# Performance work log

Measured on AMD Instinct MI355X. Metric: run time of the kernel, lower is better.

## Reference

```python
import jax, jax.numpy as jnp
import numpy as np

B, D_MODEL, C, T = 2, 256, 64, 1024
N_HEADS = 8
EPS = 1e-5


def setup_inputs() -> dict:
    key = jax.random.key(0)
    k1, k2, k3 = jax.random.split(key, 3)
    x = jax.random.normal(k1, (B, D_MODEL, C, T), dtype=jnp.float32)
    in_w = jax.random.normal(k2, (3 * D_MODEL, D_MODEL), dtype=jnp.float32) * 0.05
    in_b = jnp.zeros((3 * D_MODEL,), jnp.float32)
    out_w = jax.random.normal(k3, (D_MODEL, D_MODEL), dtype=jnp.float32) * 0.05
    out_b = jnp.zeros((D_MODEL,), jnp.float32)
    return dict(x=x, in_w=in_w, in_b=in_b, out_w=out_w, out_b=out_b)


def reference(x, in_w, in_b, out_w, out_b):
    b, d, c, t = x.shape
    h = N_HEADS
    f = d // h
    scale = 1.0 / np.sqrt(f).astype(np.float32)

    # InstanceNorm2d (no affine): normalize each (b, channel) over spatial (c, t)
    mu = x.mean(axis=(2, 3), keepdims=True)
    var = x.var(axis=(2, 3), keepdims=True)  # biased, as torch
    xn = (x - mu) / jnp.sqrt(var + EPS)

    # 1x1 conv d -> 3d
    qkv = jnp.einsum('bdct,ed->bect', xn, in_w) + in_b[None, :, None, None]
    q, k, v = jnp.split(qkv, 3, axis=1)

    def to_heads(u):
        # b (h f) c t -> (b c) h f t
        u = u.reshape(b, h, f, c, t)
        u = u.transpose(0, 3, 1, 2, 4)
        return u.reshape(b * c, h, f, t)

    q = jax.nn.softmax(to_heads(q), axis=-2) * scale  # softmax over feature dim
    k = jax.nn.softmax(to_heads(k), axis=-1)          # softmax over length dim
    v = to_heads(v) / t

    # context: [n, h, f_k, f_v]
    ctx = jnp.einsum('nhkl,nhvl->nhkv', k, v)
    out = jnp.einsum('nhdv,nhdl->nhvl', ctx, q)

    # (b c) h f t -> b (h f) c t
    out = out.reshape(b, c, h, f, t).transpose(0, 2, 3, 1, 4).reshape(b, d, c, t)

    out = jnp.einsum('bdct,ed->bect', out, out_w) + out_b[None, :, None, None]
    return out + x
```

## Files before the change

kernel.cpp:

```cpp
#include <hip/hip_runtime.h>
#include <stdint.h>

#define D_MODEL 256
#define TDIM    1024
#define NHEADS  8
#define FDIM    32
#define P_LEN   65536
#define K3      768
#define BK      64

using u16 = unsigned short;

typedef __bf16 bf16x8 __attribute__((ext_vector_type(8)));
typedef float  floatx4 __attribute__((ext_vector_type(4)));

__device__ __forceinline__ float b2f(u16 u) {
    union { float f; uint32_t i; } v; v.i = ((uint32_t)u) << 16; return v.f;
}
__device__ __forceinline__ float b2f_lo(uint32_t u) {
    union { float f; uint32_t i; } v; v.i = u << 16; return v.f;
}
__device__ __forceinline__ float b2f_hi(uint32_t u) {
    union { float f; uint32_t i; } v; v.i = u & 0xffff0000u; return v.f;
}
__device__ __forceinline__ u16 f2b(float f) {
    union { float f; uint32_t i; } v; v.f = f;
    uint32_t i = v.i;
    uint32_t r = i + 0x7fffu + ((i >> 16) & 1u);
    return (u16)(r >> 16);
}
__device__ __forceinline__ uint32_t pack2(float lo, float hi) {
    return ((uint32_t)f2b(hi) << 16) | (uint32_t)f2b(lo);
}

__device__ __forceinline__ void gload_lds16(const u16* g, u16* l) {
    __builtin_amdgcn_global_load_lds((const __attribute__((address_space(1))) void*)g,
                                     (__attribute__((address_space(3))) void*)l,
                                     16, 0, 0);
}

__device__ __forceinline__ void stc(u16* p, float v) { *p = f2b(v); }
__device__ __forceinline__ void stc(float* p, float v) { *p = v; }

__global__ __launch_bounds__(256) void stats_kernel(const float* __restrict__ x,
                                                    float* __restrict__ mu,
                                                    float* __restrict__ rstd) {
    int bd = blockIdx.x;
    const float* row = x + (size_t)bd * P_LEN;
    int tid = threadIdx.x;
    float s = 0.f, sq = 0.f;
    for (int i = 0; i < P_LEN / (256 * 4); ++i) {
        int idx = (i * 256 + tid) * 4;
        float4 u = *(const float4*)(row + idx);
        s += u.x + u.y + u.z + u.w;
        sq += u.x * u.x + u.y * u.y + u.z * u.z + u.w * u.w;
    }
    for (int off = 32; off; off >>= 1) { s += __shfl_down(s, off); sq += __shfl_down(sq, off); }
    __shared__ float rs[4], rq[4];
    if ((tid & 63) == 0) { rs[tid >> 6] = s; rq[tid >> 6] = sq; }
    __syncthreads();
    if (tid == 0) {
        float S = rs[0] + rs[1] + rs[2] + rs[3];
        float Q = rq[0] + rq[1] + rq[2] + rq[3];
        float m = S * (1.f / 65536.f);
        float var = Q * (1.f / 65536.f) - m * m;
        mu[bd] = m;
        rstd[bd] = rsqrtf(var + 1e-5f);
    }
}

__global__ __launch_bounds__(256) void fold_kernel(const float* __restrict__ in_w,
                                                   const float* __restrict__ in_b,
                                                   const float* __restrict__ mu,
                                                   const float* __restrict__ rstd,
                                                   u16* __restrict__ Wp,
                                                   float* __restrict__ bprime) {
    int bid = blockIdx.x;
    int b = bid / K3, e = bid % K3;
    int d = threadIdx.x;
    float w = in_w[e * D_MODEL + d];
    float r = rstd[b * D_MODEL + d];
    float m = mu[b * D_MODEL + d];
    Wp[(size_t)bid * D_MODEL + d] = f2b(w * r);
    float contrib = w * r * m;
    for (int off = 32; off; off >>= 1) contrib += __shfl_down(contrib, off);
    __shared__ float rr[4];
    if ((d & 63) == 0) rr[d >> 6] = contrib;
    __syncthreads();
    if (d == 0) bprime[bid] = in_b[e] - (rr[0] + rr[1] + rr[2] + rr[3]);
}

__global__ __launch_bounds__(256) void transpose_x(const float* __restrict__ x,
                                                   u16* __restrict__ xt) {
    __shared__ float tile[64][65];
    int p0 = blockIdx.x * 64;
    int d0 = blockIdx.y * 64;
    int tid = threadIdx.x;
    int dr = tid >> 4;
    int pc = (tid & 15) * 4;
#pragma unroll
    for (int it = 0; it < 4; ++it) {
        int d = it * 16 + dr;
        float4 v = *(const float4*)&x[(size_t)(d0 + d) * P_LEN + p0 + pc];
        tile[pc + 0][d] = v.x;
        tile[pc + 1][d] = v.y;
        tile[pc + 2][d] = v.z;
        tile[pc + 3][d] = v.w;
    }
    __syncthreads();
    int pr = tid >> 3;
    int dc = (tid & 7) * 8;
#pragma unroll
    for (int it = 0; it < 2; ++it) {
        int p = it * 32 + pr;
        ushort4 o0 = make_ushort4(f2b(tile[p][dc + 0]), f2b(tile[p][dc + 1]),
                                  f2b(tile[p][dc + 2]), f2b(tile[p][dc + 3]));
        ushort4 o1 = make_ushort4(f2b(tile[p][dc + 4]), f2b(tile[p][dc + 5]),
                                  f2b(tile[p][dc + 6]), f2b(tile[p][dc + 7]));
        u16* dst = xt + (size_t)(p0 + p) * D_MODEL + d0 + dc;
        *(ushort4*)dst = o0;
        *(ushort4*)(dst + 4) = o1;
    }
}

template <bool RESID, bool PERC, typename OT>
__global__ __launch_bounds__(256) void mgemm(const u16* __restrict__ A,
                                             const u16* __restrict__ Bt,
                                             const float* __restrict__ bias,
                                             const float* __restrict__ resid,
                                             OT* __restrict__ Cout) {
    __shared__ __align__(16) u16 As[128 * BK];
    __shared__ __align__(16) u16 Bs[128 * BK];
    const int tid  = threadIdx.x;
    const int wave = tid >> 6;
    const int lane = tid & 63;
    const int m0 = blockIdx.y * 128;
    const int p0 = blockIdx.x * 128;
    const int mw = (wave >> 1) * 64;
    const int nw = (wave & 1) * 64;

    const u16* Ab = PERC ? A + ((size_t)(blockIdx.x >> 3) << 16) : A;

    floatx4 acc[4][4];
#pragma unroll
    for (int i = 0; i < 4; ++i)
#pragma unroll
        for (int j = 0; j < 4; ++j) acc[i][j] = (floatx4){0.f, 0.f, 0.f, 0.f};

    const int srow = lane >> 3;
    const int schunk = lane & 7;
    const int q  = lane >> 4;
    const int rl = lane & 15;

    for (int s = 0; s < 4; ++s) {
        const int k0 = s * BK;
#pragma unroll
        for (int j = 0; j < 4; ++j) {
            int rbase = wave * 32 + j * 8;
            int r = rbase + srow;
            int cg = schunk ^ (r & 7);
            gload_lds16(Ab + ((size_t)(m0 + r) << 8) + k0 + cg * 8, &As[rbase * BK]);
            gload_lds16(Bt + ((size_t)(p0 + r) << 8) + k0 + cg * 8, &Bs[rbase * BK]);
        }
        __syncthreads();
#pragma unroll
        for (int ks = 0; ks < 2; ++ks) {
            bf16x8 af[4], bf[4];
#pragma unroll
            for (int ti = 0; ti < 4; ++ti) {
                int r = mw + 16 * ti + rl;
                int cp = (ks * 4 + q) ^ (r & 7);
                af[ti] = *(const bf16x8*)&As[r * BK + cp * 8];
            }
#pragma unroll
            for (int tj = 0; tj < 4; ++tj) {
                int r = nw + 16 * tj + rl;
                int cp = (ks * 4 + q) ^ (r & 7);
                bf[tj] = *(const bf16x8*)&Bs[r * BK + cp * 8];
            }
#pragma unroll
            for (int ti = 0; ti < 4; ++ti)
#pragma unroll
                for (int tj = 0; tj < 4; ++tj)
                    acc[ti][tj] = __builtin_amdgcn_mfma_f32_16x16x32_bf16(
                        af[ti], bf[tj], acc[ti][tj], 0, 0, 0);
        }
        __syncthreads();
    }

#pragma unroll
    for (int ti = 0; ti < 4; ++ti) {
#pragma unroll
        for (int i = 0; i < 4; ++i) {
            int e = m0 + mw + 16 * ti + 4 * q + i;
            float bv = bias[e];
            size_t rowbase = (size_t)e * P_LEN + p0 + nw;
#pragma unroll
            for (int tj = 0; tj < 4; ++tj) {
                size_t addr = rowbase + 16 * tj + rl;
                float v = acc[ti][tj][i] + bv;
                if (RESID) v += resid[addr];
                stc(Cout + addr, v);
            }
        }
    }
}

__global__ __launch_bounds__(256) void qsm_kernel(const u16* __restrict__ qkv,
                                                  u16* __restrict__ pq) {
    int tid = threadIdx.x;
    int pair = tid >> 2;
    int hq = tid & 3;
    size_t p = (size_t)blockIdx.x * 128 + (size_t)pair * 2;
    const u16* qb = qkv + p;
#pragma unroll
    for (int hi = 0; hi < 2; ++hi) {
        int h = hq * 2 + hi;
        const u16* qh = qb + (size_t)(h * FDIM) * P_LEN;
        float a[32], b[32];
#pragma unroll
        for (int f = 0; f < 32; ++f) {
            uint32_t uu = *(const uint32_t*)(qh + (size_t)f * P_LEN);
            a[f] = __expf(b2f_lo(uu));
            b[f] = __expf(b2f_hi(uu));
        }
        float sa = 0.f, sb = 0.f;
#pragma unroll
        for (int f = 0; f < 32; ++f) { sa += a[f]; sb += b[f]; }
        sa = 1.f / sa; sb = 1.f / sb;
        u16* o1 = pq + p * D_MODEL + h * FDIM;
        u16* o2 = o1 + D_MODEL;
#pragma unroll
        for (int c = 0; c < 4; ++c) {
            union { u16 u[8]; uint4 v4; } pka, pkb;
#pragma unroll
            for (int i = 0; i < 8; ++i) {
                pka.u[i] = f2b(a[c * 8 + i] * sa);
                pkb.u[i] = f2b(b[c * 8 + i] * sb);
            }
            *(uint4*)(o1 + c * 8) = pka.v4;
            *(uint4*)(o2 + c * 8) = pkb.v4;
        }
    }
}

__global__ __launch_bounds__(256) void ctx_kernel(const u16* __restrict__ qkv,
                                                  float* __restrict__ ctx) {
    int bid = blockIdx.x;
    int c = bid >> 3, h = bid & 7;
    int tid = threadIdx.x;
    size_t colbase = (size_t)c * TDIM;
    const u16* kb = qkv + (size_t)(D_MODEL + h * FDIM) * P_LEN + colbase;
    const u16* vb = qkv + (size_t)(2 * D_MODEL + h * FDIM) * P_LEN + colbase;

    __shared__ float kinv[32];
    __shared__ __align__(16) u16 ekt[32 * 264];
    __shared__ __align__(16) u16 vsb[32 * 264];

    {
        int row = tid >> 3, g = tid & 7;
        const u16* krow = kb + (size_t)row * P_LEN;
        float s = 0.f;
#pragma unroll
        for (int i = 0; i < 16; ++i) {
            uint4 u = *(const uint4*)(krow + g * 8 + i * 64);
            s += __expf(b2f_lo(u.x)) + __expf(b2f_hi(u.x))
               + __expf(b2f_lo(u.y)) + __expf(b2f_hi(u.y))
               + __expf(b2f_lo(u.z)) + __expf(b2f_hi(u.z))
               + __expf(b2f_lo(u.w)) + __expf(b2f_hi(u.w));
        }
        for (int off = 4; off; off >>= 1) s += __shfl_down(s, off, 8);
        if (g == 0) kinv[row] = 0.17677669529663687f / (s * 1024.f);
    }
    __syncthreads();

    const int lane = tid & 63;
    const int wave = tid >> 6;
    const int rl = lane & 15, q = lane >> 4;
    const int mi = wave >> 1, ni = wave & 1;
    const int o  = tid & 31;
    const int r8 = tid >> 5;
    floatx4 acc = {0.f, 0.f, 0.f, 0.f};

    for (int ch = 0; ch < 4; ++ch) {
        int t0 = ch * 256;
        if (ch) __syncthreads();
#pragma unroll
        for (int pass = 0; pass < 4; ++pass) {
            int r = pass * 8 + r8;
            float iv = kinv[r];
            uint4 u = *((const uint4*)(kb + (size_t)r * P_LEN + t0) + o);
            uint4 w = *((const uint4*)(vb + (size_t)r * P_LEN + t0) + o);
            uint4 E;
            E.x = pack2(__expf(b2f_lo(u.x)) * iv, __expf(b2f_hi(u.x)) * iv);
            E.y = pack2(__expf(b2f_lo(u.y)) * iv, __expf(b2f_hi(u.y)) * iv);
            E.z = pack2(__expf(b2f_lo(u.z)) * iv, __expf(b2f_hi(u.z)) * iv);
            E.w = pack2(__expf(b2f_lo(u.w)) * iv, __expf(b2f_hi(u.w)) * iv);
            *(uint4*)&ekt[r * 264 + o * 8] = E;
            *(uint4*)&vsb[r * 264 + o * 8] = w;
        }
        __syncthreads();
#pragma unroll
        for (int ks = 0; ks < 8; ++ks) {
            bf16x8 a  = *(const bf16x8*)&ekt[(16 * mi + rl) * 264 + ks * 32 + q * 8];
            bf16x8 bv = *(const bf16x8*)&vsb[(16 * ni + rl) * 264 + ks * 32 + q * 8];
            acc = __builtin_amdgcn_mfma_f32_16x16x32_bf16(a, bv, acc, 0, 0, 0);
        }
    }

    float* co = ctx + (size_t)bid * 1024;
#pragma unroll
    for (int i = 0; i < 4; ++i)
        co[(16 * mi + 4 * q + i) * 32 + 16 * ni + rl] = acc[i];
}

__global__ __launch_bounds__(256) void wfold_kernel(const float* __restrict__ w2,
                                                    const float* __restrict__ ctx,
                                                    u16* __restrict__ w2p) {
    __shared__ float cs[8192];
    int c = blockIdx.x;
    int tid = threadIdx.x;
    const float4* cb = (const float4*)(ctx + (size_t)c * 8192);
#pragma unroll
    for (int i = 0; i < 8; ++i)
        ((float4*)cs)[i * 256 + tid] = cb[i * 256 + tid];
    __syncthreads();
    int e = blockIdx.y * 128 + (tid >> 1);
    int hh = tid & 1;
    const float* wrow = w2 + (size_t)e * 256;
    u16* orow = w2p + ((size_t)c << 16) + (size_t)e * 256;
#pragma unroll
    for (int hi = 0; hi < 4; ++hi) {
        int h = hh * 4 + hi;
        float w[32];
#pragma unroll
        for (int v = 0; v < 8; ++v) {
            float4 t4 = *(const float4*)&wrow[h * 32 + v * 4];
            w[v * 4 + 0] = t4.x; w[v * 4 + 1] = t4.y;
            w[v * 4 + 2] = t4.z; w[v * 4 + 3] = t4.w;
        }
        const float* chp = cs + h * 1024;
#pragma unroll
        for (int kc = 0; kc < 4; ++kc) {
            union { u16 u[8]; uint4 v4; } pk;
#pragma unroll
            for (int ki = 0; ki < 8; ++ki) {
                const float* ck = chp + (kc * 8 + ki) * 32;
                float acc = 0.f;
#pragma unroll
                for (int v = 0; v < 32; v += 4) {
                    float4 c4 = *(const float4*)&ck[v];
                    acc += w[v] * c4.x + w[v + 1] * c4.y
                         + w[v + 2] * c4.z + w[v + 3] * c4.w;
                }
                pk.u[ki] = f2b(acc);
            }
            *(uint4*)(orow + h * 32 + kc * 8) = pk.v4;
        }
    }
}

extern "C" void kernel_launch(void* const* d_in, const int* in_sizes, int n_in,
                              void* d_out, int out_size, void* d_ws, size_t ws_size,
                              hipStream_t stream) {
    const float* x     = (const float*)d_in[0];
    const float* in_w  = (const float*)d_in[1];
    const float* in_b  = (const float*)d_in[2];
    const float* out_w = (const float*)d_in[3];
    const float* out_b = (const float*)d_in[4];
    float* out = (float*)d_out;

    char* ws = (char*)d_ws;
    float* mu     = (float*)(ws);
    float* rstd   = (float*)(ws + 2048);
    u16*   Wp     = (u16*)(ws + 4096);
    float* bprime = (float*)(ws + 790528);
    u16*   tbuf   = (u16*)(ws + 796672);
    u16*   qkvb   = (u16*)(ws + 34351104);
    float* ctxb   = (float*)(ws + 34351104);
    u16*   w2p    = (u16*)(ws + 34351104 + 4194304);

    stats_kernel<<<512, 256, 0, stream>>>(x, mu, rstd);
    fold_kernel<<<1536, 256, 0, stream>>>(in_w, in_b, mu, rstd, Wp, bprime);

    for (int b = 0; b < 2; ++b) {
        const float* xb = x + (size_t)b * D_MODEL * P_LEN;
        transpose_x<<<dim3(1024, 4), 256, 0, stream>>>(xb, tbuf);
        mgemm<false, false, u16><<<dim3(512, 6), 256, 0, stream>>>(
            Wp + (size_t)b * K3 * D_MODEL, tbuf, bprime + b * K3, nullptr, qkvb);
        qsm_kernel<<<512, 256, 0, stream>>>(qkvb, tbuf);
        ctx_kernel<<<512, 256, 0, stream>>>(qkvb, ctxb);
        wfold_kernel<<<dim3(64, 2), 256, 0, stream>>>(out_w, ctxb, w2p);
        mgemm<true, true, float><<<dim3(512, 2), 256, 0, stream>>>(
            w2p, tbuf, out_b, xb, out + (size_t)b * D_MODEL * P_LEN);
    }
}
```

Before: 611.8 us.

## Fuse instance-norm stats into transpose and query softmax into QKV GEMM epilogue

The separate stats pass over x is removed: the transpose kernel now accumulates per-channel sum and sum-of-squares with atomics, and the fold kernel derives mean and rstd per batch. The query feature-softmax is moved into the QKV GEMM epilogue for the first two row tiles, writing the transposed normalized q directly and removing qsm_kernel along with its reread of q. This saves one full read of x and one q round trip, at the cost of atomic contention, one-pass variance precision, and the q output now sharing qkvb's unused space.

```diff
diff --git a/kernel.cpp b/kernel.cpp
--- a/kernel.cpp
+++ b/kernel.cpp
@@ -42,56 +42,14 @@
 __device__ __forceinline__ void stc(u16* p, float v) { *p = f2b(v); }
 __device__ __forceinline__ void stc(float* p, float v) { *p = v; }
 
-__global__ __launch_bounds__(256) void stats_kernel(const float* __restrict__ x,
-                                                    float* __restrict__ mu,
-                                                    float* __restrict__ rstd) {
-    int bd = blockIdx.x;
-    const float* row = x + (size_t)bd * P_LEN;
-    int tid = threadIdx.x;
-    float s = 0.f, sq = 0.f;
-    for (int i = 0; i < P_LEN / (256 * 4); ++i) {
-        int idx = (i * 256 + tid) * 4;
-        float4 u = *(const float4*)(row + idx);
-        s += u.x + u.y + u.z + u.w;
-        sq += u.x * u.x + u.y * u.y + u.z * u.z + u.w * u.w;
-    }
-    for (int off = 32; off; off >>= 1) { s += __shfl_down(s, off); sq += __shfl_down(sq, off); }
-    __shared__ float rs[4], rq[4];
-    if ((tid & 63) == 0) { rs[tid >> 6] = s; rq[tid >> 6] = sq; }
-    __syncthreads();
-    if (tid == 0) {
-        float S = rs[0] + rs[1] + rs[2] + rs[3];
-        float Q = rq[0] + rq[1] + rq[2] + rq[3];
-        float m = S * (1.f / 65536.f);
-        float var = Q * (1.f / 65536.f) - m * m;
-        mu[bd] = m;
-        rstd[bd] = rsqrtf(var + 1e-5f);
-    }
-}
-
-__global__ __launch_bounds__(256) void fold_kernel(const float* __restrict__ in_w,
-                                                   const float* __restrict__ in_b,
-                                                   const float* __restrict__ mu,
-                                                   const float* __restrict__ rstd,
-                                                   u16* __restrict__ Wp,
-                                                   float* __restrict__ bprime) {
-    int bid = blockIdx.x;
-    int b = bid / K3, e = bid % K3;
-    int d = threadIdx.x;
-    float w = in_w[e * D_MODEL + d];
-    float r = rstd[b * D_MODEL + d];
-    float m = mu[b * D_MODEL + d];
-    Wp[(size_t)bid * D_MODEL + d] = f2b(w * r);
-    float contrib = w * r * m;
-    for (int off = 32; off; off >>= 1) contrib += __shfl_down(contrib, off);
-    __shared__ float rr[4];
-    if ((d & 63) == 0) rr[d >> 6] = contrib;
-    __syncthreads();
-    if (d == 0) bprime[bid] = in_b[e] - (rr[0] + rr[1] + rr[2] + rr[3]);
+__global__ __launch_bounds__(256) void zero_kernel(float* __restrict__ p) {
+    p[blockIdx.x * 256 + threadIdx.x] = 0.f;
 }
 
 __global__ __launch_bounds__(256) void transpose_x(const float* __restrict__ x,
-                                                   u16* __restrict__ xt) {
+                                                   u16* __restrict__ xt,
+                                                   float* __restrict__ sacc,
+                                                   float* __restrict__ qacc) {
     __shared__ float tile[64][65];
     int p0 = blockIdx.x * 64;
     int d0 = blockIdx.y * 64;
@@ -106,6 +64,17 @@
         tile[pc + 1][d] = v.y;
         tile[pc + 2][d] = v.z;
         tile[pc + 3][d] = v.w;
+        float s = v.x + v.y + v.z + v.w;
+        float sq = v.x * v.x + v.y * v.y + v.z * v.z + v.w * v.w;
+#pragma unroll
+        for (int off = 8; off; off >>= 1) {
+            s  += __shfl_down(s, off, 16);
+            sq += __shfl_down(sq, off, 16);
+        }
+        if ((tid & 15) == 0) {
+            atomicAdd(&sacc[d0 + d], s);
+            atomicAdd(&qacc[d0 + d], sq);
+        }
     }
     __syncthreads();
     int pr = tid >> 3;
@@ -123,12 +92,34 @@
     }
 }
 
-template <bool RESID, bool PERC, typename OT>
+__global__ __launch_bounds__(256) void fold_kernel(const float* __restrict__ in_w,
+                                                   const float* __restrict__ in_b,
+                                                   const float* __restrict__ sacc,
+                                                   const float* __restrict__ qacc,
+                                                   u16* __restrict__ Wp,
+                                                   float* __restrict__ bprime) {
+    int e = blockIdx.x;
+    int d = threadIdx.x;
+    float m = sacc[d] * (1.f / 65536.f);
+    float var = qacc[d] * (1.f / 65536.f) - m * m;
+    float r = rsqrtf(var + 1e-5f);
+    float w = in_w[e * D_MODEL + d];
+    Wp[(size_t)e * D_MODEL + d] = f2b(w * r);
+    float contrib = w * r * m;
+    for (int off = 32; off; off >>= 1) contrib += __shfl_down(contrib, off);
+    __shared__ float rr[4];
+    if ((d & 63) == 0) rr[d >> 6] = contrib;
+    __syncthreads();
+    if (d == 0) bprime[e] = in_b[e] - (rr[0] + rr[1] + rr[2] + rr[3]);
+}
+
+template <bool RESID, bool PERC, bool QSM, typename OT>
 __global__ __launch_bounds__(256) void mgemm(const u16* __restrict__ A,
                                              const u16* __restrict__ Bt,
                                              const float* __restrict__ bias,
                                              const float* __restrict__ resid,
-                                             OT* __restrict__ Cout) {
+                                             OT* __restrict__ Cout,
+                                             u16* __restrict__ qout) {
     __shared__ __align__(16) u16 As[128 * BK];
     __shared__ __align__(16) u16 Bs[128 * BK];
     const int tid  = threadIdx.x;
@@ -188,6 +179,47 @@
         __syncthreads();
     }
 
+    if (QSM && blockIdx.y < 2) {
+        float den[2][4] = {{0.f, 0.f, 0.f, 0.f}, {0.f, 0.f, 0.f, 0.f}};
+#pragma unroll
+        for (int ti = 0; ti < 4; ++ti) {
+#pragma unroll
+            for (int i = 0; i < 4; ++i) {
+                int e = m0 + mw + 16 * ti + 4 * q + i;
+                float bv = bias[e];
+#pragma unroll
+                for (int tj = 0; tj < 4; ++tj) {
+                    float ex = __expf(acc[ti][tj][i] + bv);
+                    acc[ti][tj][i] = ex;
+                    den[ti >> 1][tj] += ex;
+                }
+            }
+        }
+#pragma unroll
+        for (int hh = 0; hh < 2; ++hh)
+#pragma unroll
+            for (int tj = 0; tj < 4; ++tj) {
+                float dsum = den[hh][tj];
+                dsum += __shfl_xor(dsum, 16);
+                dsum += __shfl_xor(dsum, 32);
+                den[hh][tj] = 1.f / dsum;
+            }
+#pragma unroll
+        for (int tj = 0; tj < 4; ++tj) {
+            size_t p = (size_t)(p0 + nw + 16 * tj + rl);
+            u16* row = qout + p * D_MODEL + m0 + mw;
+#pragma unroll
+            for (int ti = 0; ti < 4; ++ti) {
+                float inv = den[ti >> 1][tj];
+                ushort4 o = make_ushort4(f2b(acc[ti][tj][0] * inv),
+                                         f2b(acc[ti][tj][1] * inv),
+                                         f2b(acc[ti][tj][2] * inv),
+                                         f2b(acc[ti][tj][3] * inv));
+                *(ushort4*)(row + 16 * ti + 4 * q) = o;
+            }
+        }
+        return;
+    }
 #pragma unroll
     for (int ti = 0; ti < 4; ++ti) {
 #pragma unroll
@@ -202,44 +234,6 @@
                 if (RESID) v += resid[addr];
                 stc(Cout + addr, v);
             }
-        }
-    }
-}
-
-__global__ __launch_bounds__(256) void qsm_kernel(const u16* __restrict__ qkv,
-                                                  u16* __restrict__ pq) {
-    int tid = threadIdx.x;
-    int pair = tid >> 2;
-    int hq = tid & 3;
-    size_t p = (size_t)blockIdx.x * 128 + (size_t)pair * 2;
-    const u16* qb = qkv + p;
-#pragma unroll
-    for (int hi = 0; hi < 2; ++hi) {
-        int h = hq * 2 + hi;
-        const u16* qh = qb + (size_t)(h * FDIM) * P_LEN;
-        float a[32], b[32];
-#pragma unroll
-        for (int f = 0; f < 32; ++f) {
-            uint32_t uu = *(const uint32_t*)(qh + (size_t)f * P_LEN);
-            a[f] = __expf(b2f_lo(uu));
-            b[f] = __expf(b2f_hi(uu));
-        }
-        float sa = 0.f, sb = 0.f;
-#pragma unroll
-        for (int f = 0; f < 32; ++f) { sa += a[f]; sb += b[f]; }
-        sa = 1.f / sa; sb = 1.f / sb;
-        u16* o1 = pq + p * D_MODEL + h * FDIM;
-        u16* o2 = o1 + D_MODEL;
-#pragma unroll
-        for (int c = 0; c < 4; ++c) {
-            union { u16 u[8]; uint4 v4; } pka, pkb;
-#pragma unroll
-            for (int i = 0; i < 8; ++i) {
-                pka.u[i] = f2b(a[c * 8 + i] * sa);
-                pkb.u[i] = f2b(b[c * 8 + i] * sb);
-            }
-            *(uint4*)(o1 + c * 8) = pka.v4;
-            *(uint4*)(o2 + c * 8) = pkb.v4;
         }
     }
 }
@@ -371,27 +365,31 @@
     float* out = (float*)d_out;
 
     char* ws = (char*)d_ws;
-    float* mu     = (float*)(ws);
-    float* rstd   = (float*)(ws + 2048);
+    float* sacc   = (float*)(ws);
+    float* qacc   = (float*)(ws + 2048);
     u16*   Wp     = (u16*)(ws + 4096);
     float* bprime = (float*)(ws + 790528);
     u16*   tbuf   = (u16*)(ws + 796672);
+    float* ctxb   = (float*)(ws + 796672);
+    u16*   w2p    = (u16*)(ws + 796672 + 2097152);
     u16*   qkvb   = (u16*)(ws + 34351104);
-    float* ctxb   = (float*)(ws + 34351104);
-    u16*   w2p    = (u16*)(ws + 34351104 + 4194304);
-
-    stats_kernel<<<512, 256, 0, stream>>>(x, mu, rstd);
-    fold_kernel<<<1536, 256, 0, stream>>>(in_w, in_b, mu, rstd, Wp, bprime);
+
+    zero_kernel<<<4, 256, 0, stream>>>(sacc);
 
     for (int b = 0; b < 2; ++b) {
         const float* xb = x + (size_t)b * D_MODEL * P_LEN;
-        transpose_x<<<dim3(1024, 4), 256, 0, stream>>>(xb, tbuf);
-        mgemm<false, false, u16><<<dim3(512, 6), 256, 0, stream>>>(
-            Wp + (size_t)b * K3 * D_MODEL, tbuf, bprime + b * K3, nullptr, qkvb);
-        qsm_kernel<<<512, 256, 0, stream>>>(qkvb, tbuf);
+        transpose_x<<<dim3(1024, 4), 256, 0, stream>>>(xb, tbuf,
+                                                       sacc + b * 256, qacc + b * 256);
+        fold_kernel<<<K3, 256, 0, stream>>>(in_w, in_b, sacc + b * 256,
+                                            qacc + b * 256,
+                                            Wp + (size_t)b * K3 * D_MODEL,
+                                            bprime + b * K3);
+        mgemm<false, false, true, u16><<<dim3(512, 6), 256, 0, stream>>>(
+            Wp + (size_t)b * K3 * D_MODEL, tbuf, bprime + b * K3, nullptr,
+            qkvb, qkvb );
         ctx_kernel<<<512, 256, 0, stream>>>(qkvb, ctxb);
         wfold_kernel<<<dim3(64, 2), 256, 0, stream>>>(out_w, ctxb, w2p);
-        mgemm<true, true, float><<<dim3(512, 2), 256, 0, stream>>>(
-            w2p, tbuf, out_b, xb, out + (size_t)b * D_MODEL * P_LEN);
-    }
-}
+        mgemm<true, true, false, float><<<dim3(512, 2), 256, 0, stream>>>(
+            w2p, qkvb , out_b, xb, out + (size_t)b * D_MODEL * P_LEN, nullptr);
+    }
+}
```

Result: slower. 891.7 us (+45.7%).
